# Kernel optimization log

Measured on AMD Instinct MI355X. Metric: run time of the kernel, lower is better.

Reference implementation:

```python
import jax, jax.numpy as jnp
import numpy as np

B, L, H, V = 16, 512, 256, 32000
HALF = H // 2
EPS_LN = 1e-5
EPS_NORM = 1e-12


def setup_inputs() -> dict:
    key = jax.random.key(0)
    ks = jax.random.split(key, 9)
    s = 0.02
    return {
        "seq": jax.random.randint(ks[0], (B, L), 0, V),
        "embed": jax.random.normal(ks[1], (V, H), jnp.float32) * s,
        "W1": jax.random.normal(ks[2], (2 * H, H), jnp.float32) * s,
        "b1": jnp.zeros((2 * H,), jnp.float32),
        "W2": jax.random.normal(ks[3], (H, 2 * H), jnp.float32) * s,
        "b2": jnp.zeros((H,), jnp.float32),
        "gamma": jnp.ones((H,), jnp.float32),
        "beta": jnp.zeros((H,), jnp.float32),
        "W_sem": jax.random.normal(ks[4], (HALF, H), jnp.float32) * s,
        "W_epi": jax.random.normal(ks[5], (HALF, H), jnp.float32) * s,
        "W_rp": jax.random.normal(ks[6], (H, H), jnp.float32) * s,
        "b_rp": jnp.zeros((H,), jnp.float32),
        "W_out": jax.random.normal(ks[7], (V, H), jnp.float32) * s,
        "b_out": jnp.zeros((V,), jnp.float32),
    }


def _l2norm(x):
    # F.normalize(dim=-1): x / max(||x||, eps)
    n = jnp.sqrt(jnp.sum(x * x, axis=-1, keepdims=True))
    return x / jnp.maximum(n, EPS_NORM)


def reference(seq, embed, W1, b1, W2, b2, gamma, beta, W_sem, W_epi, W_rp, b_rp, W_out, b_out):
    h = embed[seq]                                   # [B, L, H]
    ff = jnp.maximum(h @ W1.T + b1, 0.0) @ W2.T + b2  # MLP with 2H hidden
    x = h + ff
    mu = jnp.mean(x, axis=-1, keepdims=True)
    var = jnp.var(x, axis=-1, keepdims=True)
    h = (x - mu) / jnp.sqrt(var + EPS_LN) * gamma + beta  # LayerNorm

    ks_all = jnp.einsum('blh,kh->blk', h, W_sem)     # [B, L, HALF]
    ke_all = jnp.einsum('blh,kh->blk', h, W_epi)

    def step(carry, kv):
        M_s, M_e = carry
        k_s, k_e = kv                                 # [B, HALF] each
        kns = _l2norm(k_s)
        kne = _l2norm(k_e)
        vps = jnp.einsum('bij,bj->bi', M_s, kns)      # read from fast weights
        vpe = jnp.einsum('bij,bj->bi', M_e, kne)
        M_s = M_s + jnp.einsum('bi,bj->bij', k_s - vps, kns)  # delta-rule write
        M_e = M_e + jnp.einsum('bi,bj->bij', k_e - vpe, kne)
        return (M_s, M_e), None

    M0 = jnp.zeros((B, HALF, HALF), h.dtype)
    # scan over timesteps 0..L-2 (time-major)
    (M_s, M_e), _ = jax.lax.scan(
        step, (M0, M0),
        (jnp.swapaxes(ks_all[:, :-1], 0, 1), jnp.swapaxes(ke_all[:, :-1], 0, 1)))

    cs = jnp.einsum('bij,bj->bi', M_s, ks_all[:, -1])  # read with last-token query
    ce = jnp.einsum('bij,bj->bi', M_e, ke_all[:, -1])
    c = jnp.concatenate([cs, ce], axis=-1)             # [B, H]
    r = c @ W_rp.T + b_rp
    return r @ W_out.T + b_out                          # [B, V]
```

## Files before the change

kernel.cpp:

```cpp
#include <hip/hip_runtime.h>

#define B_ 16
#define L_ 512
#define H_ 256
#define V_ 32000
#define HALF_ 128

typedef __attribute__((ext_vector_type(8))) short short8;
typedef __attribute__((ext_vector_type(4))) float floatx4;

__device__ __forceinline__ unsigned short f2bf(float x) {
  unsigned int u = __float_as_uint(x);
  unsigned int r = (u + 0x7FFFu + ((u >> 16) & 1u)) >> 16;
  return (unsigned short)r;
}

__global__ void gather_kernel(const int* __restrict__ seq, const float* __restrict__ embed,
                              float* __restrict__ h, unsigned short* __restrict__ hbf) {
  int token = blockIdx.x;
  int lane = threadIdx.x;
  int row = seq[token];
  float4 v = ((const float4*)(embed + (size_t)row * H_))[lane];
  ((float4*)(h + (size_t)token * H_))[lane] = v;
  ushort4 b;
  b.x = f2bf(v.x); b.y = f2bf(v.y); b.z = f2bf(v.z); b.w = f2bf(v.w);
  *(ushort4*)(hbf + (size_t)token * H_ + lane * 4) = b;
}

__global__ void wconv_kernel(const float* __restrict__ W1, const float* __restrict__ W2,
                             const float* __restrict__ Ws, const float* __restrict__ We,
                             unsigned short* __restrict__ W1b, unsigned short* __restrict__ W2b,
                             unsigned short* __restrict__ Wcb) {
  int i = blockIdx.x * 256 + threadIdx.x;
  if (i < 131072) W1b[i] = f2bf(W1[i]);
  else if (i < 262144) W2b[i - 131072] = f2bf(W2[i - 131072]);
  else if (i < 294912) Wcb[i - 262144] = f2bf(Ws[i - 262144]);
  else Wcb[i - 262144] = f2bf(We[i - 294912]);
}

template <bool RELU, bool BIAS, bool RES, bool OUT_BF16>
__global__ __launch_bounds__(256) void gemm_mfma(const unsigned short* __restrict__ A,
                                                 const unsigned short* __restrict__ Bw,
                                                 const float* __restrict__ bias,
                                                 const float* __restrict__ Res,
                                                 float* __restrict__ Cf,
                                                 unsigned short* __restrict__ Cb,
                                                 int M, int N, int K) {
  __shared__ unsigned short As[128 * 40];
  __shared__ unsigned short Bs[128 * 40];
  int tid = threadIdx.x;
  int wave = tid >> 6, lane = tid & 63;
  int wm = (wave >> 1) * 64, wn = (wave & 1) * 64;
  int quad = lane >> 4, l15 = lane & 15;
  int bm = blockIdx.y * 128, bn = blockIdx.x * 128;
  int sr = tid >> 2, sq = tid & 3;

  floatx4 zero = {0.f, 0.f, 0.f, 0.f};
  floatx4 acc[4][4];
#pragma unroll
  for (int fi = 0; fi < 4; fi++)
#pragma unroll
    for (int fj = 0; fj < 4; fj++) acc[fi][fj] = zero;

  for (int k0 = 0; k0 < K; k0 += 32) {
    uint4 av0 = *(const uint4*)(A + (size_t)(bm + sr) * K + k0 + sq * 8);
    uint4 av1 = *(const uint4*)(A + (size_t)(bm + 64 + sr) * K + k0 + sq * 8);
    uint4 bv0 = *(const uint4*)(Bw + (size_t)(bn + sr) * K + k0 + sq * 8);
    uint4 bv1 = *(const uint4*)(Bw + (size_t)(bn + 64 + sr) * K + k0 + sq * 8);
    __syncthreads();
    *(uint4*)(As + sr * 40 + sq * 8) = av0;
    *(uint4*)(As + (64 + sr) * 40 + sq * 8) = av1;
    *(uint4*)(Bs + sr * 40 + sq * 8) = bv0;
    *(uint4*)(Bs + (64 + sr) * 40 + sq * 8) = bv1;
    __syncthreads();
    short8 af[4], bf[4];
#pragma unroll
    for (int f = 0; f < 4; f++) {
      af[f] = *(const short8*)(As + (wm + f * 16 + l15) * 40 + quad * 8);
      bf[f] = *(const short8*)(Bs + (wn + f * 16 + l15) * 40 + quad * 8);
    }
#pragma unroll
    for (int fi = 0; fi < 4; fi++)
#pragma unroll
      for (int fj = 0; fj < 4; fj++)
        acc[fi][fj] = __builtin_amdgcn_mfma_f32_16x16x32_bf16(af[fi], bf[fj], acc[fi][fj], 0, 0, 0);
  }

#pragma unroll
  for (int fi = 0; fi < 4; fi++) {
#pragma unroll
    for (int fj = 0; fj < 4; fj++) {
      int col = bn + wn + fj * 16 + l15;
      float bb = BIAS ? bias[col] : 0.f;
#pragma unroll
      for (int rg = 0; rg < 4; rg++) {
        int row = bm + wm + fi * 16 + quad * 4 + rg;
        float v = acc[fi][fj][rg] + bb;
        if (RES) v += Res[(size_t)row * N + col];
        if (RELU) v = fmaxf(v, 0.f);
        if (OUT_BF16) Cb[(size_t)row * N + col] = f2bf(v);
        else Cf[(size_t)row * N + col] = v;
      }
    }
  }
}

__global__ void ln_kernel(const float* __restrict__ x, const float* __restrict__ gamma,
                          const float* __restrict__ beta, unsigned short* __restrict__ yb) {
  int row = blockIdx.x;
  int lane = threadIdx.x;
  float4 v = ((const float4*)(x + (size_t)row * H_))[lane];
  float s = v.x + v.y + v.z + v.w;
  float sq = v.x * v.x + v.y * v.y + v.z * v.z + v.w * v.w;
#pragma unroll
  for (int off = 32; off >= 1; off >>= 1) {
    s += __shfl_xor(s, off);
    sq += __shfl_xor(sq, off);
  }
  float mu = s * (1.f / H_);
  float var = sq * (1.f / H_) - mu * mu;
  float inv = rsqrtf(var + 1e-5f);
  float4 g = ((const float4*)gamma)[lane];
  float4 b = ((const float4*)beta)[lane];
  ushort4 o;
  o.x = f2bf((v.x - mu) * inv * g.x + b.x);
  o.y = f2bf((v.y - mu) * inv * g.y + b.y);
  o.z = f2bf((v.z - mu) * inv * g.z + b.z);
  o.w = f2bf((v.w - mu) * inv * g.w + b.w);
  *(ushort4*)(yb + (size_t)row * H_ + lane * 4) = o;
}

__global__ __launch_bounds__(256) void normalize_kernel(const float* __restrict__ kcat,
                                                        unsigned short* __restrict__ khat) {
  int e = blockIdx.x * 4 + (threadIdx.x >> 6);
  int lane = threadIdx.x & 63;
  int idxm = e >> 9, t = e & 511;
  int b = idxm >> 1, mat = idxm & 1;
  const float* kp = kcat + ((size_t)b * L_ + t) * 256 + mat * 128;
  float2 v = ((const float2*)kp)[lane];
  float s = v.x * v.x + v.y * v.y;
#pragma unroll
  for (int off = 32; off >= 1; off >>= 1) s += __shfl_xor(s, off);
  float inv = 1.f / fmaxf(sqrtf(s), 1e-12f);
  ushort2 o;
  o.x = f2bf(v.x * inv);
  o.y = f2bf(v.y * inv);
  *(ushort2*)(khat + (size_t)e * HALF_ + lane * 2) = o;
}

template <int CTRL>
__device__ __forceinline__ float dpp_xor_add(float x) {
  int y = __builtin_amdgcn_mov_dpp(__float_as_int(x), CTRL, 0xf, 0xf, true);
  return x + __int_as_float(y);
}

#define BL_(u) __uint_as_float((u) << 16)
#define BH_(u) __uint_as_float((u) & 0xffff0000u)

#define SCAN_STEP(PK, PR)                                              \
  do {                                                                 \
    float k0 = BL_(PK.x), k1 = BH_(PK.x), k2 = BL_(PK.y), k3 = BH_(PK.y), \
          k4 = BL_(PK.z), k5 = BH_(PK.z), k6 = BL_(PK.w), k7 = BH_(PK.w); \
    float pa = m[0] * k0 + m[1] * k1, pb = m[2] * k2 + m[3] * k3,      \
          pc = m[4] * k4 + m[5] * k5, pd = m[6] * k6 + m[7] * k7;      \
    float p = (pa + pb) + (pc + pd);                                   \
    p = dpp_xor_add<0xB1>(p);                                          \
    p = dpp_xor_add<0x4E>(p);                                          \
    p = dpp_xor_add<0x141>(p);                                         \
    p = dpp_xor_add<0x140>(p);                                         \
    float sS = PR - p;                                                 \
    m[0] += sS * k0; m[1] += sS * k1; m[2] += sS * k2; m[3] += sS * k3; \
    m[4] += sS * k4; m[5] += sS * k5; m[6] += sS * k6; m[7] += sS * k7; \
  } while (0)

__global__ __launch_bounds__(256) void scan_kernel(const float* __restrict__ kcat,
                                                   const unsigned short* __restrict__ khat,
                                                   float* __restrict__ c) {
  int bid = blockIdx.x;
  int idxm = bid & 31;
  int rg = bid >> 5;
  int b = idxm >> 1, mat = idxm & 1;
  const unsigned short* kh = khat + (size_t)idxm * L_ * HALF_;
  const float* kbase = kcat + (size_t)b * L_ * 256 + mat * HALF_;

  int tid = threadIdx.x;
  int seg = tid & 15;
  int rl = tid >> 4;
  int r = rg * 16 + rl;
  int c0 = seg * 8;
  const float* krow = kbase + r;

  float m[8];
#pragma unroll
  for (int g = 0; g < 8; g++) m[g] = 0.f;

  uint4 pk[4];
  float pr[4];
#pragma unroll
  for (int u = 0; u < 4; u++) {
    pk[u] = *(const uint4*)(kh + (size_t)u * HALF_ + c0);
    pr[u] = krow[(size_t)u * 256];
  }

  for (int t = 0; t < 508; t += 4) {
#pragma unroll
    for (int u = 0; u < 4; u++) {
      int tt = t + u;
      uint4 nk = *(const uint4*)(kh + (size_t)(tt + 4) * HALF_ + c0);
      float nr = krow[(size_t)(tt + 4) * 256];
      SCAN_STEP(pk[u], pr[u]);
      pk[u] = nk;
      pr[u] = nr;
    }
  }
  SCAN_STEP(pk[0], pr[0]);
  SCAN_STEP(pk[1], pr[1]);
  SCAN_STEP(pk[2], pr[2]);

  float4 qa = *(const float4*)(kbase + (size_t)511 * 256 + c0);
  float4 qb = *(const float4*)(kbase + (size_t)511 * 256 + c0 + 4);
  float pa = m[0] * qa.x + m[1] * qa.y, pb2 = m[2] * qa.z + m[3] * qa.w;
  float pc = m[4] * qb.x + m[5] * qb.y, pd = m[6] * qb.z + m[7] * qb.w;
  float p = (pa + pb2) + (pc + pd);
  p = dpp_xor_add<0xB1>(p);
  p = dpp_xor_add<0x4E>(p);
  p = dpp_xor_add<0x141>(p);
  p = dpp_xor_add<0x140>(p);
  if (seg == 0) c[(size_t)b * H_ + mat * HALF_ + r] = p;
}

__global__ void rp_kernel(const float* __restrict__ c, const float* __restrict__ Wrp,
                          const float* __restrict__ brp, float* __restrict__ r) {
  int b = blockIdx.x;
  int n = threadIdx.x;
  __shared__ float cs[H_];
  cs[n] = c[(size_t)b * H_ + n];
  __syncthreads();
  const float4* w4 = (const float4*)(Wrp + (size_t)n * H_);
  const float4* c4 = (const float4*)cs;
  float acc = 0.f;
#pragma unroll 8
  for (int k = 0; k < H_ / 4; k++) {
    float4 w = w4[k], cc = c4[k];
    acc += w.x * cc.x + w.y * cc.y + w.z * cc.z + w.w * cc.w;
  }
  r[(size_t)b * H_ + n] = acc + brp[n];
}

__global__ __launch_bounds__(256) void out_kernel(const float* __restrict__ r,
                                                  const float* __restrict__ Wout,
                                                  const float* __restrict__ bout,
                                                  float* __restrict__ out) {
  __shared__ float rs[B_ * H_];
  int tid = threadIdx.x;
#pragma unroll
  for (int q = 0; q < (B_ * H_) / 256; q++) rs[q * 256 + tid] = r[q * 256 + tid];
  __syncthreads();
  int v = blockIdx.x * 256 + tid;
  const float4* w4 = (const float4*)(Wout + (size_t)v * H_);
  float acc[B_];
#pragma unroll
  for (int b = 0; b < B_; b++) acc[b] = 0.f;
  for (int k = 0; k < H_ / 4; k++) {
    float4 w = w4[k];
#pragma unroll
    for (int b = 0; b < B_; b++) {
      float4 rr = *(const float4*)&rs[b * H_ + 4 * k];
      acc[b] += w.x * rr.x + w.y * rr.y + w.z * rr.z + w.w * rr.w;
    }
  }
  float bo = bout[v];
#pragma unroll
  for (int b = 0; b < B_; b++) out[(size_t)b * V_ + v] = acc[b] + bo;
}

extern "C" void kernel_launch(void* const* d_in, const int* in_sizes, int n_in,
                              void* d_out, int out_size, void* d_ws, size_t ws_size,
                              hipStream_t stream) {
  const int* seq = (const int*)d_in[0];
  const float* embed = (const float*)d_in[1];
  const float* W1 = (const float*)d_in[2];
  const float* b1 = (const float*)d_in[3];
  const float* W2 = (const float*)d_in[4];
  const float* b2 = (const float*)d_in[5];
  const float* gamma = (const float*)d_in[6];
  const float* beta = (const float*)d_in[7];
  const float* Wsem = (const float*)d_in[8];
  const float* Wepi = (const float*)d_in[9];
  const float* Wrp = (const float*)d_in[10];
  const float* brp = (const float*)d_in[11];
  const float* Wout = (const float*)d_in[12];
  const float* bout = (const float*)d_in[13];
  float* out = (float*)d_out;

  float* ws = (float*)d_ws;
  float* h = ws;
  float* x = h;
  float* kcat = ws + 2097152;
  unsigned short* a1b = (unsigned short*)kcat;
  unsigned short* hbf = (unsigned short*)(ws + 4194304);
  unsigned short* hnb = (unsigned short*)(ws + 5242880);
  unsigned short* khat = (unsigned short*)(ws + 6291456);
  unsigned short* W1b = (unsigned short*)(ws + 7340032);
  unsigned short* W2b = (unsigned short*)(ws + 7405568);
  unsigned short* Wcb = (unsigned short*)(ws + 7471104);
  float* c = ws + 7503872;
  float* r = ws + 7508000;

  gather_kernel<<<8192, 64, 0, stream>>>(seq, embed, h, hbf);
  wconv_kernel<<<1280, 256, 0, stream>>>(W1, W2, Wsem, Wepi, W1b, W2b, Wcb);
  gemm_mfma<true, true, false, true><<<dim3(4, 64), 256, 0, stream>>>(
      hbf, W1b, b1, nullptr, nullptr, a1b, 8192, 512, 256);
  gemm_mfma<false, true, true, false><<<dim3(2, 64), 256, 0, stream>>>(
      a1b, W2b, b2, h, x, nullptr, 8192, 256, 512);
  ln_kernel<<<8192, 64, 0, stream>>>(x, gamma, beta, hnb);
  gemm_mfma<false, false, false, false><<<dim3(2, 64), 256, 0, stream>>>(
      hnb, Wcb, nullptr, nullptr, kcat, nullptr, 8192, 256, 256);
  normalize_kernel<<<4096, 256, 0, stream>>>(kcat, khat);
  scan_kernel<<<256, 256, 0, stream>>>(kcat, khat, c);
  rp_kernel<<<16, 256, 0, stream>>>(c, Wrp, brp, r);
  out_kernel<<<125, 256, 0, stream>>>(r, Wout, bout, out);
}
```

Measured before the change: 249.9 us.

## Chunk delta-rule scan via Gram matrices, fuse prep kernels, retile GEMMs and output

Adds a gram kernel that precomputes pairwise dot products of normalized keys within 4-step chunks. The scan uses these to resolve four delta-rule updates per chunk with one combined reduction phase and a small triangular solve, which shortens the serial dependency chain. The gather and weight-conversion kernels are merged into one launch. The two N=256 GEMMs use 64-row tiles to launch more blocks, and the output projection splits K across 4 lanes with padded shared memory and coalesced stores. This trades an extra kernel and some extra arithmetic for less serial latency in the scan and better occupancy elsewhere.

```diff
diff --git a/kernel.cpp b/kernel.cpp
--- a/kernel.cpp
+++ b/kernel.cpp
@@ -15,30 +15,55 @@
   return (unsigned short)r;
 }
 
-__global__ void gather_kernel(const int* __restrict__ seq, const float* __restrict__ embed,
-                              float* __restrict__ h, unsigned short* __restrict__ hbf) {
-  int token = blockIdx.x;
-  int lane = threadIdx.x;
-  int row = seq[token];
-  float4 v = ((const float4*)(embed + (size_t)row * H_))[lane];
-  ((float4*)(h + (size_t)token * H_))[lane] = v;
-  ushort4 b;
-  b.x = f2bf(v.x); b.y = f2bf(v.y); b.z = f2bf(v.z); b.w = f2bf(v.w);
-  *(ushort4*)(hbf + (size_t)token * H_ + lane * 4) = b;
-}
-
-__global__ void wconv_kernel(const float* __restrict__ W1, const float* __restrict__ W2,
-                             const float* __restrict__ Ws, const float* __restrict__ We,
-                             unsigned short* __restrict__ W1b, unsigned short* __restrict__ W2b,
-                             unsigned short* __restrict__ Wcb) {
-  int i = blockIdx.x * 256 + threadIdx.x;
-  if (i < 131072) W1b[i] = f2bf(W1[i]);
-  else if (i < 262144) W2b[i - 131072] = f2bf(W2[i - 131072]);
-  else if (i < 294912) Wcb[i - 262144] = f2bf(Ws[i - 262144]);
-  else Wcb[i - 262144] = f2bf(We[i - 294912]);
-}
-
-template <bool RELU, bool BIAS, bool RES, bool OUT_BF16>
+#define BL_(u) __uint_as_float((u) << 16)
+#define BH_(u) __uint_as_float((u) & 0xffff0000u)
+
+template <int CTRL>
+__device__ __forceinline__ float dpp_xor_add(float x) {
+  int y = __builtin_amdgcn_mov_dpp(__float_as_int(x), CTRL, 0xf, 0xf, true);
+  return x + __int_as_float(y);
+}
+
+__device__ __forceinline__ float redu16(float p) {
+  p = dpp_xor_add<0xB1>(p);
+  p = dpp_xor_add<0x4E>(p);
+  p = dpp_xor_add<0x141>(p);
+  p = dpp_xor_add<0x140>(p);
+  return p;
+}
+
+__global__ __launch_bounds__(256) void prep_kernel(const int* __restrict__ seq,
+                                                   const float* __restrict__ embed,
+                                                   float* __restrict__ h,
+                                                   unsigned short* __restrict__ hbf,
+                                                   const float* __restrict__ W1,
+                                                   const float* __restrict__ W2,
+                                                   const float* __restrict__ Ws,
+                                                   const float* __restrict__ We,
+                                                   unsigned short* __restrict__ W1b,
+                                                   unsigned short* __restrict__ W2b,
+                                                   unsigned short* __restrict__ Wcb) {
+  int blk = blockIdx.x;
+  int tid = threadIdx.x;
+  if (blk < 2048) {
+    int token = blk * 4 + (tid >> 6);
+    int lane = tid & 63;
+    int row = seq[token];
+    float4 v = ((const float4*)(embed + (size_t)row * H_))[lane];
+    ((float4*)(h + (size_t)token * H_))[lane] = v;
+    ushort4 o;
+    o.x = f2bf(v.x); o.y = f2bf(v.y); o.z = f2bf(v.z); o.w = f2bf(v.w);
+    *(ushort4*)(hbf + (size_t)token * H_ + lane * 4) = o;
+  } else {
+    int i = (blk - 2048) * 256 + tid;
+    if (i < 131072) W1b[i] = f2bf(W1[i]);
+    else if (i < 262144) W2b[i - 131072] = f2bf(W2[i - 131072]);
+    else if (i < 294912) Wcb[i - 262144] = f2bf(Ws[i - 262144]);
+    else Wcb[i - 262144] = f2bf(We[i - 294912]);
+  }
+}
+
+template <int MT, bool RELU, bool BIAS, bool RES, bool OUT_BF16>
 __global__ __launch_bounds__(256) void gemm_mfma(const unsigned short* __restrict__ A,
                                                  const unsigned short* __restrict__ Bw,
                                                  const float* __restrict__ bias,
@@ -46,48 +71,49 @@
                                                  float* __restrict__ Cf,
                                                  unsigned short* __restrict__ Cb,
                                                  int M, int N, int K) {
-  __shared__ unsigned short As[128 * 40];
+  constexpr int FI = MT / 32;
+  __shared__ unsigned short As[MT * 40];
   __shared__ unsigned short Bs[128 * 40];
   int tid = threadIdx.x;
   int wave = tid >> 6, lane = tid & 63;
-  int wm = (wave >> 1) * 64, wn = (wave & 1) * 64;
+  int wm = (wave >> 1) * (MT / 2), wn = (wave & 1) * 64;
   int quad = lane >> 4, l15 = lane & 15;
-  int bm = blockIdx.y * 128, bn = blockIdx.x * 128;
+  int bm = blockIdx.y * MT, bn = blockIdx.x * 128;
   int sr = tid >> 2, sq = tid & 3;
 
   floatx4 zero = {0.f, 0.f, 0.f, 0.f};
-  floatx4 acc[4][4];
-#pragma unroll
-  for (int fi = 0; fi < 4; fi++)
+  floatx4 acc[FI][4];
+#pragma unroll
+  for (int fi = 0; fi < FI; fi++)
 #pragma unroll
     for (int fj = 0; fj < 4; fj++) acc[fi][fj] = zero;
 
   for (int k0 = 0; k0 < K; k0 += 32) {
     uint4 av0 = *(const uint4*)(A + (size_t)(bm + sr) * K + k0 + sq * 8);
-    uint4 av1 = *(const uint4*)(A + (size_t)(bm + 64 + sr) * K + k0 + sq * 8);
+    uint4 av1;
+    if (MT == 128) av1 = *(const uint4*)(A + (size_t)(bm + 64 + sr) * K + k0 + sq * 8);
     uint4 bv0 = *(const uint4*)(Bw + (size_t)(bn + sr) * K + k0 + sq * 8);
     uint4 bv1 = *(const uint4*)(Bw + (size_t)(bn + 64 + sr) * K + k0 + sq * 8);
     __syncthreads();
     *(uint4*)(As + sr * 40 + sq * 8) = av0;
-    *(uint4*)(As + (64 + sr) * 40 + sq * 8) = av1;
+    if (MT == 128) *(uint4*)(As + (64 + sr) * 40 + sq * 8) = av1;
     *(uint4*)(Bs + sr * 40 + sq * 8) = bv0;
     *(uint4*)(Bs + (64 + sr) * 40 + sq * 8) = bv1;
     __syncthreads();
-    short8 af[4], bf[4];
-#pragma unroll
-    for (int f = 0; f < 4; f++) {
-      af[f] = *(const short8*)(As + (wm + f * 16 + l15) * 40 + quad * 8);
-      bf[f] = *(const short8*)(Bs + (wn + f * 16 + l15) * 40 + quad * 8);
-    }
-#pragma unroll
-    for (int fi = 0; fi < 4; fi++)
+    short8 af[FI], bf[4];
+#pragma unroll
+    for (int f = 0; f < FI; f++) af[f] = *(const short8*)(As + (wm + f * 16 + l15) * 40 + quad * 8);
+#pragma unroll
+    for (int f = 0; f < 4; f++) bf[f] = *(const short8*)(Bs + (wn + f * 16 + l15) * 40 + quad * 8);
+#pragma unroll
+    for (int fi = 0; fi < FI; fi++)
 #pragma unroll
       for (int fj = 0; fj < 4; fj++)
         acc[fi][fj] = __builtin_amdgcn_mfma_f32_16x16x32_bf16(af[fi], bf[fj], acc[fi][fj], 0, 0, 0);
   }
 
 #pragma unroll
-  for (int fi = 0; fi < 4; fi++) {
+  for (int fi = 0; fi < FI; fi++) {
 #pragma unroll
     for (int fj = 0; fj < 4; fj++) {
       int col = bn + wn + fj * 16 + l15;
@@ -148,33 +174,67 @@
   *(ushort2*)(khat + (size_t)e * HALF_ + lane * 2) = o;
 }
 
-template <int CTRL>
-__device__ __forceinline__ float dpp_xor_add(float x) {
-  int y = __builtin_amdgcn_mov_dpp(__float_as_int(x), CTRL, 0xf, 0xf, true);
-  return x + __int_as_float(y);
-}
-
-#define BL_(u) __uint_as_float((u) << 16)
-#define BH_(u) __uint_as_float((u) & 0xffff0000u)
-
-#define SCAN_STEP(PK, PR)                                              \
-  do {                                                                 \
-    float k0 = BL_(PK.x), k1 = BH_(PK.x), k2 = BL_(PK.y), k3 = BH_(PK.y), \
-          k4 = BL_(PK.z), k5 = BH_(PK.z), k6 = BL_(PK.w), k7 = BH_(PK.w); \
-    float pa = m[0] * k0 + m[1] * k1, pb = m[2] * k2 + m[3] * k3,      \
-          pc = m[4] * k4 + m[5] * k5, pd = m[6] * k6 + m[7] * k7;      \
-    float p = (pa + pb) + (pc + pd);                                   \
-    p = dpp_xor_add<0xB1>(p);                                          \
-    p = dpp_xor_add<0x4E>(p);                                          \
-    p = dpp_xor_add<0x141>(p);                                         \
-    p = dpp_xor_add<0x140>(p);                                         \
-    float sS = PR - p;                                                 \
-    m[0] += sS * k0; m[1] += sS * k1; m[2] += sS * k2; m[3] += sS * k3; \
-    m[4] += sS * k4; m[5] += sS * k5; m[6] += sS * k6; m[7] += sS * k7; \
+__global__ __launch_bounds__(256) void gram_kernel(const unsigned short* __restrict__ khat,
+                                                   float* __restrict__ gram) {
+  int e = blockIdx.x * 4 + (threadIdx.x >> 6);
+  int lane = threadIdx.x & 63;
+  int idxm = e >> 7, ch = e & 127;
+  const unsigned short* kp = khat + ((size_t)idxm * L_ + ch * 4) * HALF_ + lane * 2;
+  float2 a[4];
+#pragma unroll
+  for (int i = 0; i < 4; i++) {
+    unsigned int w = *(const unsigned int*)(kp + i * HALF_);
+    a[i].x = BL_(w);
+    a[i].y = BH_(w);
+  }
+  float s01 = a[0].x * a[1].x + a[0].y * a[1].y;
+  float s02 = a[0].x * a[2].x + a[0].y * a[2].y;
+  float s03 = a[0].x * a[3].x + a[0].y * a[3].y;
+  float s12 = a[1].x * a[2].x + a[1].y * a[2].y;
+  float s13 = a[1].x * a[3].x + a[1].y * a[3].y;
+  float s23 = a[2].x * a[3].x + a[2].y * a[3].y;
+#pragma unroll
+  for (int off = 32; off >= 1; off >>= 1) {
+    s01 += __shfl_xor(s01, off);
+    s02 += __shfl_xor(s02, off);
+    s03 += __shfl_xor(s03, off);
+    s12 += __shfl_xor(s12, off);
+    s13 += __shfl_xor(s13, off);
+    s23 += __shfl_xor(s23, off);
+  }
+  if (lane == 0) {
+    float4 g0 = {s01, s02, s03, s12};
+    float2 g1 = {s13, s23};
+    *(float4*)(gram + (size_t)e * 8) = g0;
+    *(float2*)(gram + (size_t)e * 8 + 4) = g1;
+  }
+}
+
+#define UNPK(P, K)                                                         \
+  float K##0 = BL_(P.x), K##1 = BH_(P.x), K##2 = BL_(P.y), K##3 = BH_(P.y), \
+        K##4 = BL_(P.z), K##5 = BH_(P.z), K##6 = BL_(P.w), K##7 = BH_(P.w);
+
+#define DOT8(K, OUT)                                                     \
+  float OUT;                                                             \
+  {                                                                      \
+    float a_ = m[0] * K##0 + m[1] * K##1, b_ = m[2] * K##2 + m[3] * K##3, \
+          c_ = m[4] * K##4 + m[5] * K##5, d_ = m[6] * K##6 + m[7] * K##7; \
+    OUT = (a_ + b_) + (c_ + d_);                                         \
+  }
+
+#define SCAN_STEP(PK, PR)                                                \
+  do {                                                                   \
+    UNPK(PK, kz)                                                         \
+    DOT8(kz, p_)                                                         \
+    p_ = redu16(p_);                                                     \
+    float sS = PR - p_;                                                  \
+    m[0] += sS * kz0; m[1] += sS * kz1; m[2] += sS * kz2; m[3] += sS * kz3; \
+    m[4] += sS * kz4; m[5] += sS * kz5; m[6] += sS * kz6; m[7] += sS * kz7; \
   } while (0)
 
 __global__ __launch_bounds__(256) void scan_kernel(const float* __restrict__ kcat,
                                                    const unsigned short* __restrict__ khat,
+                                                   const float* __restrict__ gram,
                                                    float* __restrict__ c) {
   int bid = blockIdx.x;
   int idxm = bid & 31;
@@ -182,6 +242,7 @@
   int b = idxm >> 1, mat = idxm & 1;
   const unsigned short* kh = khat + (size_t)idxm * L_ * HALF_;
   const float* kbase = kcat + (size_t)b * L_ * 256 + mat * HALF_;
+  const float* gp = gram + (size_t)idxm * 128 * 8;
 
   int tid = threadIdx.x;
   int seg = tid & 15;
@@ -194,38 +255,60 @@
 #pragma unroll
   for (int g = 0; g < 8; g++) m[g] = 0.f;
 
-  uint4 pk[4];
-  float pr[4];
-#pragma unroll
-  for (int u = 0; u < 4; u++) {
-    pk[u] = *(const uint4*)(kh + (size_t)u * HALF_ + c0);
-    pr[u] = krow[(size_t)u * 256];
-  }
-
-  for (int t = 0; t < 508; t += 4) {
-#pragma unroll
-    for (int u = 0; u < 4; u++) {
-      int tt = t + u;
-      uint4 nk = *(const uint4*)(kh + (size_t)(tt + 4) * HALF_ + c0);
-      float nr = krow[(size_t)(tt + 4) * 256];
-      SCAN_STEP(pk[u], pr[u]);
-      pk[u] = nk;
-      pr[u] = nr;
+  uint4 pk0 = *(const uint4*)(kh + 0 * HALF_ + c0);
+  uint4 pk1 = *(const uint4*)(kh + 1 * HALF_ + c0);
+  uint4 pk2 = *(const uint4*)(kh + 2 * HALF_ + c0);
+  uint4 pk3 = *(const uint4*)(kh + 3 * HALF_ + c0);
+  float pr0 = krow[0], pr1 = krow[256], pr2 = krow[512], pr3 = krow[768];
+  float4 g03 = *(const float4*)(gp);
+  float2 g45 = *(const float2*)(gp + 4);
+
+  for (int ch = 0; ch < 127; ch++) {
+    const unsigned short* kn = kh + (size_t)(ch + 1) * 4 * HALF_ + c0;
+    uint4 n0 = *(const uint4*)(kn);
+    uint4 n1 = *(const uint4*)(kn + HALF_);
+    uint4 n2 = *(const uint4*)(kn + 2 * HALF_);
+    uint4 n3 = *(const uint4*)(kn + 3 * HALF_);
+    const float* rn = krow + (size_t)(ch + 1) * 4 * 256;
+    float nr0 = rn[0], nr1 = rn[256], nr2 = rn[512], nr3 = rn[768];
+    float4 ng03 = *(const float4*)(gp + (size_t)(ch + 1) * 8);
+    float2 ng45 = *(const float2*)(gp + (size_t)(ch + 1) * 8 + 4);
+
+    {
+      UNPK(pk0, ka) UNPK(pk1, kb) UNPK(pk2, kc) UNPK(pk3, kd)
+      DOT8(ka, p0) DOT8(kb, p1) DOT8(kc, p2) DOT8(kd, p3)
+      p0 = redu16(p0);
+      p1 = redu16(p1);
+      p2 = redu16(p2);
+      p3 = redu16(p3);
+      float d0 = pr0 - p0;
+      float d1 = pr1 - p1 - g03.x * d0;
+      float d2 = pr2 - p2 - g03.y * d0 - g03.w * d1;
+      float d3 = pr3 - p3 - g03.z * d0 - g45.x * d1 - g45.y * d2;
+      m[0] += d0 * ka0 + d1 * kb0 + d2 * kc0 + d3 * kd0;
+      m[1] += d0 * ka1 + d1 * kb1 + d2 * kc1 + d3 * kd1;
+      m[2] += d0 * ka2 + d1 * kb2 + d2 * kc2 + d3 * kd2;
+      m[3] += d0 * ka3 + d1 * kb3 + d2 * kc3 + d3 * kd3;
+      m[4] += d0 * ka4 + d1 * kb4 + d2 * kc4 + d3 * kd4;
+      m[5] += d0 * ka5 + d1 * kb5 + d2 * kc5 + d3 * kd5;
+      m[6] += d0 * ka6 + d1 * kb6 + d2 * kc6 + d3 * kd6;
+      m[7] += d0 * ka7 + d1 * kb7 + d2 * kc7 + d3 * kd7;
     }
-  }
-  SCAN_STEP(pk[0], pr[0]);
-  SCAN_STEP(pk[1], pr[1]);
-  SCAN_STEP(pk[2], pr[2]);
+
+    pk0 = n0; pk1 = n1; pk2 = n2; pk3 = n3;
+    pr0 = nr0; pr1 = nr1; pr2 = nr2; pr3 = nr3;
+    g03 = ng03; g45 = ng45;
+  }
+
+  SCAN_STEP(pk0, pr0);
+  SCAN_STEP(pk1, pr1);
+  SCAN_STEP(pk2, pr2);
 
   float4 qa = *(const float4*)(kbase + (size_t)511 * 256 + c0);
   float4 qb = *(const float4*)(kbase + (size_t)511 * 256 + c0 + 4);
   float pa = m[0] * qa.x + m[1] * qa.y, pb2 = m[2] * qa.z + m[3] * qa.w;
   float pc = m[4] * qb.x + m[5] * qb.y, pd = m[6] * qb.z + m[7] * qb.w;
-  float p = (pa + pb2) + (pc + pd);
-  p = dpp_xor_add<0xB1>(p);
-  p = dpp_xor_add<0x4E>(p);
-  p = dpp_xor_add<0x141>(p);
-  p = dpp_xor_add<0x140>(p);
+  float p = redu16((pa + pb2) + (pc + pd));
   if (seg == 0) c[(size_t)b * H_ + mat * HALF_ + r] = p;
 }
 
@@ -251,27 +334,49 @@
                                                   const float* __restrict__ Wout,
                                                   const float* __restrict__ bout,
                                                   float* __restrict__ out) {
-  __shared__ float rs[B_ * H_];
+  __shared__ float rs[16 * 272];
+  __shared__ float obuf[16 * 68];
   int tid = threadIdx.x;
 #pragma unroll
-  for (int q = 0; q < (B_ * H_) / 256; q++) rs[q * 256 + tid] = r[q * 256 + tid];
+  for (int q = 0; q < 16; q++) {
+    int idx = q * 256 + tid;
+    int bb = idx >> 8, cc = idx & 255;
+    rs[bb * 272 + cc + 4 * (cc >> 6)] = r[idx];
+  }
   __syncthreads();
-  int v = blockIdx.x * 256 + tid;
-  const float4* w4 = (const float4*)(Wout + (size_t)v * H_);
-  float acc[B_];
-#pragma unroll
-  for (int b = 0; b < B_; b++) acc[b] = 0.f;
-  for (int k = 0; k < H_ / 4; k++) {
-    float4 w = w4[k];
-#pragma unroll
-    for (int b = 0; b < B_; b++) {
-      float4 rr = *(const float4*)&rs[b * H_ + 4 * k];
-      acc[b] += w.x * rr.x + w.y * rr.y + w.z * rr.z + w.w * rr.w;
+  int row = tid >> 2, part = tid & 3;
+  int v = blockIdx.x * 64 + row;
+  const float4* w4 = (const float4*)(Wout + (size_t)v * H_ + part * 64);
+  float acc[16];
+#pragma unroll
+  for (int bb = 0; bb < 16; bb++) acc[bb] = 0.f;
+#pragma unroll 4
+  for (int j = 0; j < 16; j++) {
+    float4 w = w4[j];
+#pragma unroll
+    for (int bb = 0; bb < 16; bb++) {
+      float4 rv = *(const float4*)&rs[bb * 272 + part * 68 + j * 4];
+      acc[bb] += w.x * rv.x + w.y * rv.y + w.z * rv.z + w.w * rv.w;
     }
   }
   float bo = bout[v];
 #pragma unroll
-  for (int b = 0; b < B_; b++) out[(size_t)b * V_ + v] = acc[b] + bo;
+  for (int bb = 0; bb < 16; bb++) {
+    acc[bb] = dpp_xor_add<0xB1>(acc[bb]);
+    acc[bb] = dpp_xor_add<0x4E>(acc[bb]);
+  }
+#pragma unroll
+  for (int q = 0; q < 4; q++) {
+    int bb = part * 4 + q;
+    obuf[bb * 68 + row] = acc[bb] + bo;
+  }
+  __syncthreads();
+#pragma unroll
+  for (int q = 0; q < 4; q++) {
+    int idx = q * 256 + tid;
+    int bb = idx >> 6, vl = idx & 63;
+    out[(size_t)bb * V_ + blockIdx.x * 64 + vl] = obuf[bb * 68 + vl];
+  }
 }
 
 extern "C" void kernel_launch(void* const* d_in, const int* in_sizes, int n_in,
@@ -299,6 +404,7 @@
   float* kcat = ws + 2097152;
   unsigned short* a1b = (unsigned short*)kcat;
   unsigned short* hbf = (unsigned short*)(ws + 4194304);
+  float* gram = ws + 4718592;
   unsigned short* hnb = (unsigned short*)(ws + 5242880);
   unsigned short* khat = (unsigned short*)(ws + 6291456);
   unsigned short* W1b = (unsigned short*)(ws + 7340032);
@@ -307,17 +413,17 @@
   float* c = ws + 7503872;
   float* r = ws + 7508000;
 
-  gather_kernel<<<8192, 64, 0, stream>>>(seq, embed, h, hbf);
-  wconv_kernel<<<1280, 256, 0, stream>>>(W1, W2, Wsem, Wepi, W1b, W2b, Wcb);
-  gemm_mfma<true, true, false, true><<<dim3(4, 64), 256, 0, stream>>>(
+  prep_kernel<<<3328, 256, 0, stream>>>(seq, embed, h, hbf, W1, W2, Wsem, Wepi, W1b, W2b, Wcb);
+  gemm_mfma<128, true, true, false, true><<<dim3(4, 64), 256, 0, stream>>>(
       hbf, W1b, b1, nullptr, nullptr, a1b, 8192, 512, 256);
-  gemm_mfma<false, true, true, false><<<dim3(2, 64), 256, 0, stream>>>(
+  gemm_mfma<64, false, true, true, false><<<dim3(2, 128), 256, 0, stream>>>(
       a1b, W2b, b2, h, x, nullptr, 8192, 256, 512);
   ln_kernel<<<8192, 64, 0, stream>>>(x, gamma, beta, hnb);
-  gemm_mfma<false, false, false, false><<<dim3(2, 64), 256, 0, stream>>>(
+  gemm_mfma<64, false, false, false, false><<<dim3(2, 128), 256, 0, stream>>>(
       hnb, Wcb, nullptr, nullptr, kcat, nullptr, 8192, 256, 256);
   normalize_kernel<<<4096, 256, 0, stream>>>(kcat, khat);
-  scan_kernel<<<256, 256, 0, stream>>>(kcat, khat, c);
+  gram_kernel<<<1024, 256, 0, stream>>>(khat, gram);
+  scan_kernel<<<256, 256, 0, stream>>>(kcat, khat, gram, c);
   rp_kernel<<<16, 256, 0, stream>>>(c, Wrp, brp, r);
-  out_kernel<<<125, 256, 0, stream>>>(r, Wout, bout, out);
-}
+  out_kernel<<<500, 256, 0, stream>>>(r, Wout, bout, out);
+}
```

After: 271.7 us. +8.7%, slower.
